# Optimization experiments

Hardware: AMD Instinct MI355X
Metric: run time of the kernel (lower is better)

## Reference

```python
import jax, jax.numpy as jnp
import numpy as np

B, S, H, R = 64, 2048, 512, 256
NEG = -1.0e9


def setup_inputs() -> dict:
    key = jax.random.key(0)
    ks = jax.random.split(key, 12)
    sc_h = 1.0 / np.sqrt(H)
    sc_r = 1.0 / np.sqrt(R)
    return {
        "sent_h": jax.random.normal(ks[0], (B, S, H), jnp.float32),
        "rel": jax.random.normal(ks[1], (B, R), jnp.float32),
        "pool": jax.random.normal(ks[2], (B, H), jnp.float32),
        "mask": jax.random.randint(ks[3], (B, S), 0, 2, jnp.int32),
        "Wg_w": jax.random.normal(ks[4], (H, H), jnp.float32) * sc_h,
        "Wg_b": jnp.zeros((H,), jnp.float32),
        "Wh_w": jax.random.normal(ks[5], (H, H), jnp.float32) * sc_h,
        "Wh_b": jnp.zeros((H,), jnp.float32),
        "Wr_w": jax.random.normal(ks[6], (H, R), jnp.float32) * sc_r,
        "Wr_b": jnp.zeros((H,), jnp.float32),
        "alpha_w": jax.random.normal(ks[7], (1, H), jnp.float32) * sc_h,
        "alpha_b": jnp.zeros((1,), jnp.float32),
    }


def reference(sent_h, rel, pool, mask, Wg_w, Wg_b, Wh_w, Wh_b, Wr_w, Wr_b, alpha_w, alpha_b):
    # linear projections (torch Linear: x @ W.T + b)
    relation = rel @ Wr_w.T + Wr_b          # [B, H]
    sent = jnp.einsum('bsh,kh->bsk', sent_h, Wh_w) + Wh_b  # [B, S, H]
    global_sen = pool @ Wg_w.T + Wg_b       # [B, H]
    mix = jnp.tanh(relation[:, None, :] + sent + global_sen[:, None, :])  # [B, S, H]
    weight = jnp.einsum('bsh,h->bs', mix, alpha_w[0]) + alpha_b[0]        # [B, S]
    weight = jnp.where(mask == 0, NEG, weight)
    weight_ = jax.nn.softmax(weight, axis=-1)
    att_res = jnp.einsum('bs,bsh->bh', weight_, sent)  # [B, H]
    return (att_res, weight_)
```

## Files before the change

### kernel.cpp

```cpp
#include <hip/hip_runtime.h>
#include <cstdint>
#include <cstddef>

#define B_ 64
#define S_ 2048
#define H_ 512
#define R_ 256
#define M_ (B_ * S_)
#define NEGV (-1.0e9f)

typedef short short8 __attribute__((ext_vector_type(8)));
typedef unsigned short u16x8 __attribute__((ext_vector_type(8)));
typedef float f32x4 __attribute__((ext_vector_type(4)));
typedef unsigned short u16;

__device__ __forceinline__ u16 f2b(float x) {
    union { float f; uint32_t u; } c; c.f = x;
    uint32_t u = c.u;
    uint32_t r = (u + 0x7fffu + ((u >> 16) & 1u)) >> 16;
    return (u16)r;
}
__device__ __forceinline__ float b2f(u16 u) {
    union { uint32_t u; float f; } c; c.u = ((uint32_t)u) << 16;
    return c.f;
}
__device__ __forceinline__ float fast_tanh(float v) {
    float e = __expf(2.0f * v);
    return 1.0f - 2.0f / (e + 1.0f);
}
__device__ __forceinline__ void load_lds16(const void* g, void* l) {
    __builtin_amdgcn_global_load_lds((__attribute__((address_space(1))) void*)g,
                                     (__attribute__((address_space(3))) void*)l,
                                     16, 0, 0);
}

__global__ void k_convert(const float* __restrict__ sent, u16* __restrict__ sentb) {
    const long n8 = (long)M_ * H_ / 8;
    long stride = (long)gridDim.x * blockDim.x;
    for (long i = (long)blockIdx.x * blockDim.x + threadIdx.x; i < n8; i += stride) {
        float4 v0 = ((const float4*)sent)[2 * i];
        float4 v1 = ((const float4*)sent)[2 * i + 1];
        u16x8 o;
        o[0] = f2b(v0.x); o[1] = f2b(v0.y); o[2] = f2b(v0.z); o[3] = f2b(v0.w);
        o[4] = f2b(v1.x); o[5] = f2b(v1.y); o[6] = f2b(v1.z); o[7] = f2b(v1.w);
        ((u16x8*)sentb)[i] = o;
    }
}

__global__ void k_base(const float* __restrict__ rel, const float* __restrict__ pool,
                       const float* __restrict__ Wg_w, const float* __restrict__ Wg_b,
                       const float* __restrict__ Wh_b,
                       const float* __restrict__ Wr_w, const float* __restrict__ Wr_b,
                       const float* __restrict__ whw, float* __restrict__ base,
                       u16* __restrict__ whwb) {
    int tid = threadIdx.x;
    {
        int gi = blockIdx.x * 256 + tid;
        float4 v = ((const float4*)whw)[gi];
        ushort4 o; o.x = f2b(v.x); o.y = f2b(v.y); o.z = f2b(v.z); o.w = f2b(v.w);
        ((ushort4*)whwb)[gi] = o;
    }
    int b = blockIdx.x >> 2, q = blockIdx.x & 3;
    __shared__ __attribute__((aligned(16))) float srel[R_];
    __shared__ __attribute__((aligned(16))) float spool[H_];
    __shared__ float accs[128];
    srel[tid & 255] = rel[b * R_ + (tid & 255)];
    for (int i = tid; i < H_; i += 256) spool[i] = pool[b * H_ + i];
    __syncthreads();
    int kk = tid & 127, half = tid >> 7;
    int k = q * 128 + kk;
    float acc = 0.f;
    if (half == 0) {
        acc = Wr_b[k] + Wg_b[k] + Wh_b[k];
        const float4* wr = (const float4*)(Wr_w + (size_t)k * R_);
        #pragma unroll 8
        for (int r4 = 0; r4 < R_ / 4; ++r4) {
            float4 w = wr[r4]; float4 x = ((const float4*)srel)[r4];
            acc += w.x * x.x + w.y * x.y + w.z * x.z + w.w * x.w;
        }
        const float4* wg = (const float4*)(Wg_w + (size_t)k * H_);
        #pragma unroll 8
        for (int h4 = 0; h4 < 32; ++h4) {
            float4 w = wg[h4]; float4 x = ((const float4*)spool)[h4];
            acc += w.x * x.x + w.y * x.y + w.z * x.z + w.w * x.w;
        }
    } else {
        const float4* wg = (const float4*)(Wg_w + (size_t)k * H_);
        #pragma unroll 8
        for (int h4 = 32; h4 < 128; ++h4) {
            float4 w = wg[h4]; float4 x = ((const float4*)spool)[h4];
            acc += w.x * x.x + w.y * x.y + w.z * x.z + w.w * x.w;
        }
    }
    if (half) accs[kk] = acc;
    __syncthreads();
    if (!half) base[b * H_ + k] = acc + accs[kk];
}

__launch_bounds__(256)
__global__ void k_gemm(const u16* __restrict__ A,
                       const u16* __restrict__ Bw,
                       const float* __restrict__ base,
                       const float* __restrict__ alpha,
                       float* __restrict__ partial)
{
    const int K = 512;
    int j = blockIdx.x;
    int xcd  = j & 7;
    int slot = j >> 3;
    int nb   = slot & 3;
    int mb   = (slot >> 2) * 8 + xcd;
    int m0 = mb * 128;
    int n0 = nb * 128;
    int b  = m0 >> 11;

    int tid = threadIdx.x;
    int w  = tid >> 6;
    int l  = tid & 63;
    int wm = w & 1, wn = w >> 1;
    int lr = l & 15;
    int lq = l >> 4;

    __shared__ u16 smA[128 * 64];
    __shared__ u16 smB[128 * 64];
    __shared__ float red[2][2][64];

    f32x4 zero = {0.f, 0.f, 0.f, 0.f};
    f32x4 acc[4][4];
    #pragma unroll
    for (int i = 0; i < 4; ++i)
        #pragma unroll
        for (int jj = 0; jj < 4; ++jj) acc[i][jj] = zero;

    for (int kt = 0; kt < 8; ++kt) {
        int k0 = kt * 64;
        #pragma unroll
        for (int i = 0; i < 4; ++i) {
            int c  = w * 4 + i;
            int mf = c >> 1, kc = c & 1;
            int row = mf * 16 + lr;
            int col = k0 + kc * 32 + lq * 8;
            const u16* ga = A  + (size_t)(m0 + row) * K + col;
            const u16* gb = Bw + (size_t)(n0 + row) * K + col;
            load_lds16(ga, smA + c * 512);
            load_lds16(gb, smB + c * 512);
        }
        __syncthreads();
        #pragma unroll
        for (int kc = 0; kc < 2; ++kc) {
            short8 af[4], bf[4];
            #pragma unroll
            for (int mi = 0; mi < 4; ++mi)
                af[mi] = *(const short8*)(smA + ((wm * 4 + mi) * 2 + kc) * 512 + l * 8);
            #pragma unroll
            for (int ni = 0; ni < 4; ++ni)
                bf[ni] = *(const short8*)(smB + ((wn * 4 + ni) * 2 + kc) * 512 + l * 8);
            #pragma unroll
            for (int mi = 0; mi < 4; ++mi)
                #pragma unroll
                for (int ni = 0; ni < 4; ++ni)
                    acc[mi][ni] = __builtin_amdgcn_mfma_f32_16x16x32_bf16(af[mi], bf[ni], acc[mi][ni], 0, 0, 0);
        }
        __syncthreads();
    }

    float basev[4], alphav[4];
    #pragma unroll
    for (int ni = 0; ni < 4; ++ni) {
        int n = n0 + wn * 64 + ni * 16 + lr;
        basev[ni]  = base[b * H_ + n];
        alphav[ni] = alpha[n];
    }
    #pragma unroll
    for (int mi = 0; mi < 4; ++mi) {
        #pragma unroll
        for (int r = 0; r < 4; ++r) {
            float s = 0.f;
            #pragma unroll
            for (int ni = 0; ni < 4; ++ni) {
                float v = acc[mi][ni][r] + basev[ni];
                s += fast_tanh(v) * alphav[ni];
            }
            s += __shfl_xor(s, 1);
            s += __shfl_xor(s, 2);
            s += __shfl_xor(s, 4);
            s += __shfl_xor(s, 8);
            if (lr == 0) red[wm][wn][mi * 16 + lq * 4 + r] = s;
        }
    }
    __syncthreads();
    if (tid < 128) {
        int wmi = tid >> 6, row = tid & 63;
        float sum = red[wmi][0][row] + red[wmi][1][row];
        partial[(size_t)nb * M_ + m0 + wmi * 64 + row] = sum;
    }
}

__global__ void k_softmax(const float* __restrict__ partial, const int* __restrict__ mask,
                          const float* __restrict__ alpha_b, float* __restrict__ wout) {
    int b = blockIdx.x;
    int tid = threadIdx.x;
    __shared__ float sred[8];
    float x[8];
    float ab = alpha_b[0];
    float lmax = -3.0e38f;
    #pragma unroll
    for (int jj = 0; jj < 8; ++jj) {
        int s = tid + jj * 256;
        size_t m = (size_t)b * S_ + s;
        float v = partial[m] + partial[(size_t)M_ + m] + partial[2 * (size_t)M_ + m] + partial[3 * (size_t)M_ + m] + ab;
        if (mask[b * S_ + s] == 0) v = NEGV;
        x[jj] = v;
        lmax = fmaxf(lmax, v);
    }
    #pragma unroll
    for (int off = 1; off < 64; off <<= 1) lmax = fmaxf(lmax, __shfl_xor(lmax, off));
    int wv = tid >> 6, l = tid & 63;
    if (l == 0) sred[wv] = lmax;
    __syncthreads();
    float gmax = fmaxf(fmaxf(sred[0], sred[1]), fmaxf(sred[2], sred[3]));
    float lsum = 0.f;
    #pragma unroll
    for (int jj = 0; jj < 8; ++jj) { x[jj] = __expf(x[jj] - gmax); lsum += x[jj]; }
    #pragma unroll
    for (int off = 1; off < 64; off <<= 1) lsum += __shfl_xor(lsum, off);
    if (l == 0) sred[4 + wv] = lsum;
    __syncthreads();
    float inv = 1.f / (sred[4] + sred[5] + sred[6] + sred[7]);
    #pragma unroll
    for (int jj = 0; jj < 8; ++jj) {
        int s = tid + jj * 256;
        wout[(size_t)b * S_ + s] = x[jj] * inv;
    }
}

__global__ void k_wsum(const u16* __restrict__ sentb, const float* __restrict__ wrow_g,
                       float* __restrict__ t) {
    int b  = blockIdx.x >> 3;
    int hc = blockIdx.x & 7;
    int tid = threadIdx.x;
    __shared__ __attribute__((aligned(16))) float wrow[S_];
    __shared__ float4 red4[256];
    ((float4*)wrow)[tid]       = ((const float4*)(wrow_g + (size_t)b * S_))[tid];
    ((float4*)wrow)[tid + 256] = ((const float4*)(wrow_g + (size_t)b * S_))[tid + 256];
    __syncthreads();
    int hi = tid & 15, sg = tid >> 4;
    const u16* bp = sentb + (size_t)b * S_ * H_ + hc * 64 + hi * 4;
    float a0 = 0.f, a1 = 0.f, a2 = 0.f, a3 = 0.f;
    for (int s0 = sg; s0 < S_; s0 += 64) {
        #pragma unroll
        for (int u = 0; u < 4; ++u) {
            int s = s0 + u * 16;
            ushort4 v = *(const ushort4*)(bp + (size_t)s * H_);
            float wgt = wrow[s];
            a0 += wgt * b2f(v.x); a1 += wgt * b2f(v.y); a2 += wgt * b2f(v.z); a3 += wgt * b2f(v.w);
        }
    }
    red4[tid] = make_float4(a0, a1, a2, a3);
    __syncthreads();
    if (tid < 16) {
        float4 sacc = red4[tid];
        #pragma unroll
        for (int g = 1; g < 16; ++g) {
            float4 o = red4[g * 16 + tid];
            sacc.x += o.x; sacc.y += o.y; sacc.z += o.z; sacc.w += o.w;
        }
        float* tp = t + (size_t)b * H_ + hc * 64 + tid * 4;
        tp[0] = sacc.x; tp[1] = sacc.y; tp[2] = sacc.z; tp[3] = sacc.w;
    }
}

__global__ void k_att(const float* __restrict__ t, const float* __restrict__ Whw,
                      const float* __restrict__ Whb, float* __restrict__ out) {
    int tid = threadIdx.x;
    int b = blockIdx.x >> 2, q = blockIdx.x & 3;
    __shared__ __attribute__((aligned(16))) float st[H_];
    __shared__ float accs[128];
    for (int i = tid; i < H_; i += 256) st[i] = t[(size_t)b * H_ + i];
    __syncthreads();
    int hh = tid & 127, half = tid >> 7;
    int h = q * 128 + hh;
    const float4* wr = (const float4*)(Whw + (size_t)h * H_) + half * 64;
    const float4* sx = (const float4*)st + half * 64;
    float acc = 0.f;
    #pragma unroll 8
    for (int i = 0; i < 64; ++i) {
        float4 w = wr[i]; float4 x = sx[i];
        acc += w.x * x.x + w.y * x.y + w.z * x.z + w.w * x.w;
    }
    if (half) accs[hh] = acc;
    __syncthreads();
    if (!half) out[(size_t)b * H_ + h] = acc + accs[hh] + Whb[h];
}

extern "C" void kernel_launch(void* const* d_in, const int* in_sizes, int n_in,
                              void* d_out, int out_size, void* d_ws, size_t ws_size,
                              hipStream_t stream) {
    const float* sent_h  = (const float*)d_in[0];
    const float* rel     = (const float*)d_in[1];
    const float* pool    = (const float*)d_in[2];
    const int*   mask    = (const int*)d_in[3];
    const float* Wg_w    = (const float*)d_in[4];
    const float* Wg_b    = (const float*)d_in[5];
    const float* Wh_w    = (const float*)d_in[6];
    const float* Wh_b    = (const float*)d_in[7];
    const float* Wr_w    = (const float*)d_in[8];
    const float* Wr_b    = (const float*)d_in[9];
    const float* alpha_w = (const float*)d_in[10];
    const float* alpha_b = (const float*)d_in[11];
    float* out = (float*)d_out;

    char* ws = (char*)d_ws;
    u16*   sentb   = (u16*)ws;
    u16*   whwb    = (u16*)(ws + 134217728);
    float* base    = (float*)(ws + 134217728 + 524288);
    float* partial = (float*)(ws + 134217728 + 524288 + 131072);
    float* tbuf    = (float*)(ws + 134217728 + 524288 + 131072 + 2097152);

    float* att_out = out;
    float* w_out   = out + B_ * H_;

    k_convert<<<dim3(4096), dim3(256), 0, stream>>>(sent_h, sentb);
    k_base<<<dim3(256), dim3(256), 0, stream>>>(rel, pool, Wg_w, Wg_b, Wh_b, Wr_w, Wr_b, Wh_w, base, whwb);
    k_gemm<<<dim3((M_ / 128) * 4), dim3(256), 0, stream>>>(sentb, whwb, base, alpha_w, partial);
    k_softmax<<<dim3(B_), dim3(256), 0, stream>>>(partial, mask, alpha_b, w_out);
    k_wsum<<<dim3(B_ * 8), dim3(256), 0, stream>>>(sentb, w_out, tbuf);
    k_att<<<dim3(256), dim3(256), 0, stream>>>(tbuf, Wh_w, Wh_b, att_out);
}
```

Measured before the change: 614.7 us.

## Restructure GEMM to direct-global loads with larger tiles and rework small kernels

Measured after the change: 690.6 us. 1.12x slower.

```diff
diff --git a/kernel.cpp b/kernel.cpp
--- a/kernel.cpp
+++ b/kernel.cpp
@@ -27,11 +27,6 @@
 __device__ __forceinline__ float fast_tanh(float v) {
     float e = __expf(2.0f * v);
     return 1.0f - 2.0f / (e + 1.0f);
-}
-__device__ __forceinline__ void load_lds16(const void* g, void* l) {
-    __builtin_amdgcn_global_load_lds((__attribute__((address_space(1))) void*)g,
-                                     (__attribute__((address_space(3))) void*)l,
-                                     16, 0, 0);
 }
 
 __global__ void k_convert(const float* __restrict__ sent, u16* __restrict__ sentb) {
@@ -53,122 +48,109 @@
                        const float* __restrict__ Wr_w, const float* __restrict__ Wr_b,
                        const float* __restrict__ whw, float* __restrict__ base,
                        u16* __restrict__ whwb) {
-    int tid = threadIdx.x;
-    {
-        int gi = blockIdx.x * 256 + tid;
+    int q = blockIdx.x;
+    int tid = threadIdx.x;
+    #pragma unroll
+    for (int u = 0; u < 4; ++u) {
+        int gi = q * 1024 + u * 256 + tid;
         float4 v = ((const float4*)whw)[gi];
         ushort4 o; o.x = f2b(v.x); o.y = f2b(v.y); o.z = f2b(v.z); o.w = f2b(v.w);
         ((ushort4*)whwb)[gi] = o;
     }
-    int b = blockIdx.x >> 2, q = blockIdx.x & 3;
-    __shared__ __attribute__((aligned(16))) float srel[R_];
-    __shared__ __attribute__((aligned(16))) float spool[H_];
-    __shared__ float accs[128];
-    srel[tid & 255] = rel[b * R_ + (tid & 255)];
-    for (int i = tid; i < H_; i += 256) spool[i] = pool[b * H_ + i];
-    __syncthreads();
-    int kk = tid & 127, half = tid >> 7;
-    int k = q * 128 + kk;
-    float acc = 0.f;
-    if (half == 0) {
-        acc = Wr_b[k] + Wg_b[k] + Wh_b[k];
-        const float4* wr = (const float4*)(Wr_w + (size_t)k * R_);
+    __shared__ __attribute__((aligned(16))) float swr[8 * 260];
+    __shared__ __attribute__((aligned(16))) float swg[8 * 516];
+    int k0 = q * 8;
+    for (int i = tid; i < 8 * 64; i += 256) {
+        int r = i >> 6, c = i & 63;
+        ((float4*)(swr + r * 260))[c] = ((const float4*)(Wr_w + (size_t)(k0 + r) * R_))[c];
+    }
+    for (int i = tid; i < 8 * 128; i += 256) {
+        int r = i >> 7, c = i & 127;
+        ((float4*)(swg + r * 516))[c] = ((const float4*)(Wg_w + (size_t)(k0 + r) * H_))[c];
+    }
+    __syncthreads();
+    int ki = tid & 7, bi0 = tid >> 3;
+    float bias = Wr_b[k0 + ki] + Wg_b[k0 + ki] + Wh_b[k0 + ki];
+    #pragma unroll
+    for (int p = 0; p < 2; ++p) {
+        int b = bi0 + p * 32;
+        float acc = bias;
+        const float4* xr = (const float4*)(rel + (size_t)b * R_);
+        const float4* wr = (const float4*)(swr + ki * 260);
         #pragma unroll 8
-        for (int r4 = 0; r4 < R_ / 4; ++r4) {
-            float4 w = wr[r4]; float4 x = ((const float4*)srel)[r4];
+        for (int i = 0; i < 64; ++i) {
+            float4 w = wr[i]; float4 x = xr[i];
             acc += w.x * x.x + w.y * x.y + w.z * x.z + w.w * x.w;
         }
-        const float4* wg = (const float4*)(Wg_w + (size_t)k * H_);
+        const float4* xg = (const float4*)(pool + (size_t)b * H_);
+        const float4* wg = (const float4*)(swg + ki * 516);
         #pragma unroll 8
-        for (int h4 = 0; h4 < 32; ++h4) {
-            float4 w = wg[h4]; float4 x = ((const float4*)spool)[h4];
+        for (int i = 0; i < 128; ++i) {
+            float4 w = wg[i]; float4 x = xg[i];
             acc += w.x * x.x + w.y * x.y + w.z * x.z + w.w * x.w;
         }
-    } else {
-        const float4* wg = (const float4*)(Wg_w + (size_t)k * H_);
-        #pragma unroll 8
-        for (int h4 = 32; h4 < 128; ++h4) {
-            float4 w = wg[h4]; float4 x = ((const float4*)spool)[h4];
-            acc += w.x * x.x + w.y * x.y + w.z * x.z + w.w * x.w;
-        }
-    }
-    if (half) accs[kk] = acc;
-    __syncthreads();
-    if (!half) base[b * H_ + k] = acc + accs[kk];
-}
-
-__launch_bounds__(256)
+        base[(size_t)b * H_ + k0 + ki] = acc;
+    }
+}
+
+__launch_bounds__(256, 2)
 __global__ void k_gemm(const u16* __restrict__ A,
                        const u16* __restrict__ Bw,
                        const float* __restrict__ base,
                        const float* __restrict__ alpha,
                        float* __restrict__ partial)
 {
-    const int K = 512;
     int j = blockIdx.x;
     int xcd  = j & 7;
     int slot = j >> 3;
     int nb   = slot & 3;
-    int mb   = (slot >> 2) * 8 + xcd;
-    int m0 = mb * 128;
+    int mbg  = (slot >> 2) * 8 + xcd;
+    int m0 = mbg * 256;
     int n0 = nb * 128;
     int b  = m0 >> 11;
 
     int tid = threadIdx.x;
     int w  = tid >> 6;
     int l  = tid & 63;
-    int wm = w & 1, wn = w >> 1;
     int lr = l & 15;
     int lq = l >> 4;
 
-    __shared__ u16 smA[128 * 64];
-    __shared__ u16 smB[128 * 64];
-    __shared__ float red[2][2][64];
+    uint32_t aoff[4], boff[8];
+    #pragma unroll
+    for (int mi = 0; mi < 4; ++mi)
+        aoff[mi] = (uint32_t)(m0 + w * 64 + mi * 16 + lr) * 512u + (uint32_t)(lq * 8);
+    #pragma unroll
+    for (int ni = 0; ni < 8; ++ni)
+        boff[ni] = (uint32_t)(n0 + ni * 16 + lr) * 512u + (uint32_t)(lq * 8);
 
     f32x4 zero = {0.f, 0.f, 0.f, 0.f};
-    f32x4 acc[4][4];
-    #pragma unroll
-    for (int i = 0; i < 4; ++i)
-        #pragma unroll
-        for (int jj = 0; jj < 4; ++jj) acc[i][jj] = zero;
-
-    for (int kt = 0; kt < 8; ++kt) {
-        int k0 = kt * 64;
-        #pragma unroll
-        for (int i = 0; i < 4; ++i) {
-            int c  = w * 4 + i;
-            int mf = c >> 1, kc = c & 1;
-            int row = mf * 16 + lr;
-            int col = k0 + kc * 32 + lq * 8;
-            const u16* ga = A  + (size_t)(m0 + row) * K + col;
-            const u16* gb = Bw + (size_t)(n0 + row) * K + col;
-            load_lds16(ga, smA + c * 512);
-            load_lds16(gb, smB + c * 512);
-        }
-        __syncthreads();
-        #pragma unroll
-        for (int kc = 0; kc < 2; ++kc) {
-            short8 af[4], bf[4];
+    f32x4 acc[4][8];
+    #pragma unroll
+    for (int mi = 0; mi < 4; ++mi)
+        #pragma unroll
+        for (int ni = 0; ni < 8; ++ni) acc[mi][ni] = zero;
+
+    #pragma unroll
+    for (int kt = 0; kt < 16; ++kt) {
+        short8 av[4], bv[8];
+        #pragma unroll
+        for (int mi = 0; mi < 4; ++mi)
+            av[mi] = *(const short8*)(A + aoff[mi] + kt * 32);
+        #pragma unroll
+        for (int ni = 0; ni < 8; ++ni)
+            bv[ni] = *(const short8*)(Bw + boff[ni] + kt * 32);
+        #pragma unroll
+        for (int mi = 0; mi < 4; ++mi)
             #pragma unroll
-            for (int mi = 0; mi < 4; ++mi)
-                af[mi] = *(const short8*)(smA + ((wm * 4 + mi) * 2 + kc) * 512 + l * 8);
-            #pragma unroll
-            for (int ni = 0; ni < 4; ++ni)
-                bf[ni] = *(const short8*)(smB + ((wn * 4 + ni) * 2 + kc) * 512 + l * 8);
-            #pragma unroll
-            for (int mi = 0; mi < 4; ++mi)
-                #pragma unroll
-                for (int ni = 0; ni < 4; ++ni)
-                    acc[mi][ni] = __builtin_amdgcn_mfma_f32_16x16x32_bf16(af[mi], bf[ni], acc[mi][ni], 0, 0, 0);
-        }
-        __syncthreads();
-    }
-
-    float basev[4], alphav[4];
-    #pragma unroll
-    for (int ni = 0; ni < 4; ++ni) {
-        int n = n0 + wn * 64 + ni * 16 + lr;
-        basev[ni]  = base[b * H_ + n];
+            for (int ni = 0; ni < 8; ++ni)
+                acc[mi][ni] = __builtin_amdgcn_mfma_f32_16x16x32_bf16(av[mi], bv[ni], acc[mi][ni], 0, 0, 0);
+    }
+
+    float basev[8], alphav[8];
+    #pragma unroll
+    for (int ni = 0; ni < 8; ++ni) {
+        int n = n0 + ni * 16 + lr;
+        basev[ni]  = base[(size_t)b * H_ + n];
         alphav[ni] = alpha[n];
     }
     #pragma unroll
@@ -177,7 +159,7 @@
         for (int r = 0; r < 4; ++r) {
             float s = 0.f;
             #pragma unroll
-            for (int ni = 0; ni < 4; ++ni) {
+            for (int ni = 0; ni < 8; ++ni) {
                 float v = acc[mi][ni][r] + basev[ni];
                 s += fast_tanh(v) * alphav[ni];
             }
@@ -185,14 +167,9 @@
             s += __shfl_xor(s, 2);
             s += __shfl_xor(s, 4);
             s += __shfl_xor(s, 8);
-            if (lr == 0) red[wm][wn][mi * 16 + lq * 4 + r] = s;
-        }
-    }
-    __syncthreads();
-    if (tid < 128) {
-        int wmi = tid >> 6, row = tid & 63;
-        float sum = red[wmi][0][row] + red[wmi][1][row];
-        partial[(size_t)nb * M_ + m0 + wmi * 64 + row] = sum;
+            if (lr == 0)
+                partial[(size_t)nb * M_ + m0 + w * 64 + mi * 16 + lq * 4 + r] = s;
+        }
     }
 }
 
@@ -236,61 +213,66 @@
 
 __global__ void k_wsum(const u16* __restrict__ sentb, const float* __restrict__ wrow_g,
                        float* __restrict__ t) {
-    int b  = blockIdx.x >> 3;
-    int hc = blockIdx.x & 7;
+    int b  = blockIdx.x >> 2;
+    int hc = blockIdx.x & 3;
     int tid = threadIdx.x;
     __shared__ __attribute__((aligned(16))) float wrow[S_];
-    __shared__ float4 red4[256];
+    __shared__ float sred[16][128];
     ((float4*)wrow)[tid]       = ((const float4*)(wrow_g + (size_t)b * S_))[tid];
     ((float4*)wrow)[tid + 256] = ((const float4*)(wrow_g + (size_t)b * S_))[tid + 256];
     __syncthreads();
     int hi = tid & 15, sg = tid >> 4;
-    const u16* bp = sentb + (size_t)b * S_ * H_ + hc * 64 + hi * 4;
-    float a0 = 0.f, a1 = 0.f, a2 = 0.f, a3 = 0.f;
-    for (int s0 = sg; s0 < S_; s0 += 64) {
-        #pragma unroll
-        for (int u = 0; u < 4; ++u) {
-            int s = s0 + u * 16;
-            ushort4 v = *(const ushort4*)(bp + (size_t)s * H_);
+    const u16* bp = sentb + (size_t)b * S_ * H_ + hc * 128 + hi * 8;
+    float a[8];
+    #pragma unroll
+    for (int jj = 0; jj < 8; ++jj) a[jj] = 0.f;
+    for (int si = 0; si < S_; si += 128) {
+        #pragma unroll
+        for (int u = 0; u < 8; ++u) {
+            int s = si + sg + u * 16;
+            u16x8 v = *(const u16x8*)(bp + (size_t)s * H_);
             float wgt = wrow[s];
-            a0 += wgt * b2f(v.x); a1 += wgt * b2f(v.y); a2 += wgt * b2f(v.z); a3 += wgt * b2f(v.w);
-        }
-    }
-    red4[tid] = make_float4(a0, a1, a2, a3);
-    __syncthreads();
-    if (tid < 16) {
-        float4 sacc = red4[tid];
-        #pragma unroll
-        for (int g = 1; g < 16; ++g) {
-            float4 o = red4[g * 16 + tid];
-            sacc.x += o.x; sacc.y += o.y; sacc.z += o.z; sacc.w += o.w;
-        }
-        float* tp = t + (size_t)b * H_ + hc * 64 + tid * 4;
-        tp[0] = sacc.x; tp[1] = sacc.y; tp[2] = sacc.z; tp[3] = sacc.w;
+            #pragma unroll
+            for (int jj = 0; jj < 8; ++jj) a[jj] += wgt * b2f(v[jj]);
+        }
+    }
+    #pragma unroll
+    for (int jj = 0; jj < 8; ++jj) sred[sg][hi * 8 + jj] = a[jj];
+    __syncthreads();
+    if (tid < 128) {
+        float s = 0.f;
+        #pragma unroll
+        for (int g = 0; g < 16; ++g) s += sred[g][tid];
+        t[(size_t)b * H_ + hc * 128 + tid] = s;
     }
 }
 
 __global__ void k_att(const float* __restrict__ t, const float* __restrict__ Whw,
                       const float* __restrict__ Whb, float* __restrict__ out) {
-    int tid = threadIdx.x;
-    int b = blockIdx.x >> 2, q = blockIdx.x & 3;
-    __shared__ __attribute__((aligned(16))) float st[H_];
-    __shared__ float accs[128];
-    for (int i = tid; i < H_; i += 256) st[i] = t[(size_t)b * H_ + i];
-    __syncthreads();
-    int hh = tid & 127, half = tid >> 7;
-    int h = q * 128 + hh;
-    const float4* wr = (const float4*)(Whw + (size_t)h * H_) + half * 64;
-    const float4* sx = (const float4*)st + half * 64;
-    float acc = 0.f;
-    #pragma unroll 8
-    for (int i = 0; i < 64; ++i) {
-        float4 w = wr[i]; float4 x = sx[i];
-        acc += w.x * x.x + w.y * x.y + w.z * x.z + w.w * x.w;
-    }
-    if (half) accs[hh] = acc;
-    __syncthreads();
-    if (!half) out[(size_t)b * H_ + h] = acc + accs[hh] + Whb[h];
+    int q = blockIdx.x;
+    int tid = threadIdx.x;
+    __shared__ __attribute__((aligned(16))) float sw[8 * 516];
+    int k0 = q * 8;
+    for (int i = tid; i < 8 * 128; i += 256) {
+        int r = i >> 7, c = i & 127;
+        ((float4*)(sw + r * 516))[c] = ((const float4*)(Whw + (size_t)(k0 + r) * H_))[c];
+    }
+    __syncthreads();
+    int ki = tid & 7, bi0 = tid >> 3;
+    float bias = Whb[k0 + ki];
+    #pragma unroll
+    for (int p = 0; p < 2; ++p) {
+        int b = bi0 + p * 32;
+        float acc = bias;
+        const float4* xv = (const float4*)(t + (size_t)b * H_);
+        const float4* wv = (const float4*)(sw + ki * 516);
+        #pragma unroll 8
+        for (int i = 0; i < 128; ++i) {
+            float4 w = wv[i]; float4 x = xv[i];
+            acc += w.x * x.x + w.y * x.y + w.z * x.z + w.w * x.w;
+        }
+        out[(size_t)b * H_ + k0 + ki] = acc;
+    }
 }
 
 extern "C" void kernel_launch(void* const* d_in, const int* in_sizes, int n_in,
@@ -320,10 +302,10 @@
     float* att_out = out;
     float* w_out   = out + B_ * H_;
 
-    k_convert<<<dim3(4096), dim3(256), 0, stream>>>(sent_h, sentb);
-    k_base<<<dim3(256), dim3(256), 0, stream>>>(rel, pool, Wg_w, Wg_b, Wh_b, Wr_w, Wr_b, Wh_w, base, whwb);
-    k_gemm<<<dim3((M_ / 128) * 4), dim3(256), 0, stream>>>(sentb, whwb, base, alpha_w, partial);
+    k_convert<<<dim3(8192), dim3(256), 0, stream>>>(sent_h, sentb);
+    k_base<<<dim3(64), dim3(256), 0, stream>>>(rel, pool, Wg_w, Wg_b, Wh_b, Wr_w, Wr_b, Wh_w, base, whwb);
+    k_gemm<<<dim3(2048), dim3(256), 0, stream>>>(sentb, whwb, base, alpha_w, partial);
     k_softmax<<<dim3(B_), dim3(256), 0, stream>>>(partial, mask, alpha_b, w_out);
-    k_wsum<<<dim3(B_ * 8), dim3(256), 0, stream>>>(sentb, w_out, tbuf);
-    k_att<<<dim3(256), dim3(256), 0, stream>>>(tbuf, Wh_w, Wh_b, att_out);
-}
+    k_wsum<<<dim3(B_ * 4), dim3(256), 0, stream>>>(sentb, w_out, tbuf);
+    k_att<<<dim3(64), dim3(256), 0, stream>>>(tbuf, Wh_w, Wh_b, att_out);
+}
```
